# Kernel tuning notes

Measured on AMD Instinct MI355X. Metric: run time of the kernel, lower is better.

The kernel has to match this reference:

```python
import jax, jax.numpy as jnp
import numpy as np

B, T, D, K = 16, 3000, 512, 3
N_TOK = 448          # static max token count (targets are <= 448)
N_MAX = N_TOK + 1    # scatter bins incl. overflow bin, matches torch n_max
LN_EPS = 1e-5


def setup_inputs() -> dict:
    key = jax.random.key(0)
    k0, k1, k2, k3, k4 = jax.random.split(key, 5)
    encoder_1d = jax.random.normal(k0, (B, T, D), jnp.float32)
    # depthwise conv kernel [D, 1, K] (torch Conv1d groups=D, no bias)
    conv_w = jax.random.normal(k1, (D, 1, K), jnp.float32) * (1.0 / np.sqrt(K))
    ln_gamma = jnp.ones((D,), jnp.float32)
    ln_beta = jnp.zeros((D,), jnp.float32)
    proj_w = jax.random.normal(k2, (D,), jnp.float32) * (1.0 / np.sqrt(D))
    alpha_init = min(2048.0 / 3000.0, 0.99)
    proj_b = jnp.float32(np.log(alpha_init / (1.0 - alpha_init)))
    input_lengths = jax.random.randint(k3, (B,), T // 2, T + 1).astype(jnp.int32)
    target_lengths = jax.random.randint(k4, (B,), 300, N_TOK + 1).astype(jnp.int32)
    return {"encoder_1d": encoder_1d, "conv_w": conv_w, "ln_gamma": ln_gamma,
            "ln_beta": ln_beta, "proj_w": proj_w, "proj_b": proj_b,
            "input_lengths": input_lengths, "target_lengths": target_lengths}


def _cif(encoder_1d, conv_w, ln_gamma, ln_beta, proj_w, proj_b,
         input_lengths, target_lengths):
    dt = encoder_1d.dtype
    # ---- weight predictor: depthwise conv + LN + linear + sigmoid ----
    x = jnp.transpose(encoder_1d, (0, 2, 1))                      # [B, D, T]
    x = jax.lax.conv_general_dilated(
        x, conv_w, window_strides=(1,), padding=[(K // 2, K // 2)],
        dimension_numbers=("NCH", "OIH", "NCH"), feature_group_count=D)
    x = jnp.transpose(x, (0, 2, 1))                               # [B, T, D]
    mu = jnp.mean(x, axis=-1, keepdims=True)
    var = jnp.mean(jnp.square(x - mu), axis=-1, keepdims=True)
    x = (x - mu) * jax.lax.rsqrt(var + LN_EPS) * ln_gamma + ln_beta
    alpha = jax.nn.sigmoid(jnp.einsum("btd,d->bt", x, proj_w) + proj_b)  # [B, T]
    # ---- padding mask ----
    valid = jnp.arange(T)[None, :] < input_lengths[:, None]
    alpha = jnp.where(valid, alpha, jnp.zeros((), dt))
    # ---- quantity loss ----
    tgt = target_lengths.astype(dt)
    sum_alpha = jnp.sum(alpha, axis=1)
    qty_loss = jnp.mean(jnp.abs(sum_alpha - tgt))
    # ---- training-mode rescale so cumsum ends exactly at target ----
    alpha_cif = alpha * (tgt / jnp.maximum(sum_alpha, 1e-8))[:, None]
    # ---- CIF integration: cumsum + two scatter-adds ----
    cum = jnp.cumsum(alpha_cif, axis=1)                           # [B, T]
    cum_prev = jnp.pad(cum[:, :-1], ((0, 0), (1, 0)))
    k_lo = jnp.floor(cum_prev).astype(jnp.int32)
    k_hi = jnp.floor(cum).astype(jnp.int32)
    boundary = (k_lo + 1).astype(dt)
    w_lo = jnp.maximum(jnp.minimum(cum, boundary) - cum_prev, 0.0)
    w_hi = jnp.maximum(cum - boundary, 0.0)
    bidx = jnp.arange(B)[:, None]                                 # [B, 1] -> bcast [B, T]
    out = jnp.zeros((B, N_MAX, D), dt)
    out = out.at[bidx, jnp.clip(k_lo, 0, N_MAX - 1)].add(encoder_1d * w_lo[..., None])
    out = out.at[bidx, jnp.clip(k_hi, 0, N_MAX - 1)].add(encoder_1d * w_hi[..., None])
    return out[:, :N_TOK], alpha, qty_loss


def reference(encoder_1d, conv_w, ln_gamma, ln_beta, proj_w, proj_b,
              input_lengths, target_lengths):
    return _cif(encoder_1d, conv_w, ln_gamma, ln_beta, proj_w, proj_b,
                input_lengths, target_lengths)
```

## Files before the change

### kernel.cpp

```cpp
#include <hip/hip_runtime.h>
#include <math.h>

#define B_ 16
#define T_ 3000
#define D_ 512
#define NTOK 448
#define LN_EPS 1e-5f

#define WS_DIFF 16
#define WS_CUM  64
#define WS_AE   (64 + B_ * T_)

struct F8 { float v[8]; };

__device__ inline F8 load8(const float* __restrict__ p) {
    F8 r;
    float4 a = *(const float4*)p;
    float4 b = *(const float4*)(p + 4);
    r.v[0]=a.x; r.v[1]=a.y; r.v[2]=a.z; r.v[3]=a.w;
    r.v[4]=b.x; r.v[5]=b.y; r.v[6]=b.z; r.v[7]=b.w;
    return r;
}

__global__ __launch_bounds__(256) void k_alpha(
    const float* __restrict__ enc, const float* __restrict__ convw,
    const float* __restrict__ gamma, const float* __restrict__ beta,
    const float* __restrict__ projw, const float* __restrict__ projb,
    const int* __restrict__ ilen, float* __restrict__ alpha_out)
{
    const int NB = 188;
    int wave = threadIdx.x >> 6;
    int lane = threadIdx.x & 63;
    int b  = blockIdx.x / NB;
    int tb = blockIdx.x % NB;
    int t0 = tb * 16 + wave * 4;
    int d0 = lane * 8;
    if (t0 >= T_) return;

    int il = ilen[b];
    if (t0 >= il) {
        if (lane == 0) {
#pragma unroll
            for (int q = 0; q < 4; ++q) {
                int t = t0 + q;
                if (t < T_) alpha_out[b * T_ + t] = 0.0f;
            }
        }
        return;
    }

    const float* rowp = enc + ((size_t)b * T_ + t0) * D_ + d0;

    F8 r[6];
#pragma unroll
    for (int i = 0; i < 6; ++i) {
        int t = t0 - 1 + i;
        if (t >= 0 && t < T_) r[i] = load8(rowp + (ptrdiff_t)(i - 1) * D_);
        else { for (int j = 0; j < 8; ++j) r[i].v[j] = 0.f; }
    }

    float w24[24];
    const float4* wp = (const float4*)(convw + (size_t)d0 * 3);
#pragma unroll
    for (int i = 0; i < 6; ++i) {
        float4 q = wp[i];
        w24[4*i+0]=q.x; w24[4*i+1]=q.y; w24[4*i+2]=q.z; w24[4*i+3]=q.w;
    }
    F8 pw = load8(projw + d0);
    F8 gm = load8(gamma + d0);
    F8 bt = load8(beta + d0);
    float pg[8];
    float c0p = 0.f, c1p = 0.f;
#pragma unroll
    for (int j = 0; j < 8; ++j) {
        pg[j] = pw.v[j] * gm.v[j];
        c0p += pw.v[j] * bt.v[j];
        c1p += pg[j];
    }

    float s1[4], s2[4], sp[4];
#pragma unroll
    for (int q = 0; q < 4; ++q) { s1[q]=0.f; s2[q]=0.f; sp[q]=0.f; }

#pragma unroll
    for (int q = 0; q < 4; ++q) {
#pragma unroll
        for (int j = 0; j < 8; ++j) {
            float y = r[q].v[j]*w24[3*j] + r[q+1].v[j]*w24[3*j+1] + r[q+2].v[j]*w24[3*j+2];
            s1[q] += y; s2[q] += y*y; sp[q] += pg[j]*y;
        }
    }
#pragma unroll
    for (int off = 1; off < 64; off <<= 1) {
#pragma unroll
        for (int q = 0; q < 4; ++q) {
            s1[q] += __shfl_xor(s1[q], off);
            s2[q] += __shfl_xor(s2[q], off);
            sp[q] += __shfl_xor(sp[q], off);
        }
        c0p += __shfl_xor(c0p, off);
        c1p += __shfl_xor(c1p, off);
    }
    if (lane == 0) {
        float c0 = c0p + projb[0];
        float c1 = c1p;
#pragma unroll
        for (int q = 0; q < 4; ++q) {
            int t = t0 + q;
            if (t >= T_) break;
            float mu  = s1[q] * (1.0f / D_);
            float var = s2[q] * (1.0f / D_) - mu * mu;
            float rsig = rsqrtf(var + LN_EPS);
            float logit = rsig * (sp[q] - mu * c1) + c0;
            float a = 1.0f / (1.0f + expf(-logit));
            if (t >= il) a = 0.0f;
            alpha_out[b * T_ + t] = a;
        }
    }
}

__global__ __launch_bounds__(512) void k_prep(
    const float* __restrict__ alpha, const int* __restrict__ tlen,
    const int* __restrict__ ilen, float* __restrict__ ws)
{
    __shared__ float sc[T_];
    __shared__ float part[8];
    __shared__ int   sstg[452];

    int b = blockIdx.x;
    int tid = threadIdx.x;
    int wave = tid >> 6;
    int lane = tid & 63;

    float* cumg = ws + WS_CUM + (size_t)b * T_;
    int2*  aeg  = (int2*)(ws + WS_AE) + b * NTOK;

    float run = 0.f;
    for (int base = 0; base < T_; base += 512) {
        int t = base + tid;
        float v = (t < T_) ? alpha[b * T_ + t] : 0.f;
#pragma unroll
        for (int off = 1; off < 64; off <<= 1) {
            float n = __shfl_up(v, off);
            if (lane >= off) v += n;
        }
        if (lane == 63) part[wave] = v;
        __syncthreads();
        float prefix = run;
        for (int w = 0; w < 8; ++w) {
            float pv = part[w];
            if (w < wave) prefix += pv;
            run += pv;
        }
        v += prefix;
        if (t < T_) sc[t] = v;
        __syncthreads();
    }

    float sum = run;
    float tgt = (float)tlen[b];
    float scale = tgt / fmaxf(sum, 1e-8f);
    if (tid == 0) ws[WS_DIFF + b] = fabsf(sum - tgt);

    for (int t = tid; t < T_; t += 512) {
        float cv = sc[t] * scale;
        sc[t] = cv;
        cumg[t] = cv;
    }
    __syncthreads();

    for (int k = tid; k < 450; k += 512) {
        float vk = (float)k;
        int lo = 0, hi = T_;
        while (lo < hi) {
            int mid = (lo + hi) >> 1;
            if (sc[mid] < vk) lo = mid + 1; else hi = mid;
        }
        sstg[k] = lo;
    }
    __syncthreads();

    int il = ilen[b];
    for (int k = tid; k < NTOK; k += 512) {
        int a = sstg[k];
        int e = sstg[k + 1] + 1;
        if (e > il) e = il;
        aeg[k] = make_int2(a, e);
    }
}

__global__ __launch_bounds__(256) void k_gather(
    const float* __restrict__ enc, const float* __restrict__ ws,
    float* __restrict__ out, float* __restrict__ qty)
{
    int bid = blockIdx.x;
    if (bid == B_ * 112) {
        int lane = threadIdx.x;
        if (lane < 64) {
            float v = (lane < B_) ? ws[WS_DIFF + lane] : 0.f;
#pragma unroll
            for (int off = 1; off < 16; off <<= 1) v += __shfl_xor(v, off);
            if (lane == 0) *qty = v * (1.0f / B_);
        }
        return;
    }

    const int NBLK = NTOK / 4;
    int b  = bid / NBLK;
    int kg = bid % NBLK;
    int wave = threadIdx.x >> 6;
    int lane = threadIdx.x & 63;
    int k = kg * 4 + wave;

    const float* cb  = ws + WS_CUM + (size_t)b * T_;
    const int2*  aeg = (const int2*)(ws + WS_AE) + b * NTOK;

    int2 ae = aeg[k];
    int a = ae.x, e = ae.y;

    int d0 = lane * 8;
    const float* encb = enc + (size_t)b * T_ * D_ + d0;

    float4 aa = {0,0,0,0}, ab = {0,0,0,0};
    float fk = (float)k;

    for (int base = a; base < e; base += 63) {
        int n = e - base; if (n > 63) n = 63;
        float cl = 0.0f;
        int t = base - 1 + lane;
        if (lane <= n && t >= 0) cl = cb[t];
        float cn = __shfl_down(cl, 1);
        float fklo = floorf(cl);
        float bnd  = fklo + 1.0f;
        float wlo  = fmaxf(fminf(cn, bnd) - cl, 0.0f);
        float whi  = fmaxf(cn - bnd, 0.0f);
        float wl = (fklo == fk ? wlo : 0.0f) + (floorf(cn) == fk ? whi : 0.0f);
        if (lane >= n) wl = 0.0f;

#pragma unroll 4
        for (int j = 0; j < n; ++j) {
            float w = __shfl(wl, j);
            const float* rp = encb + (size_t)(base + j) * D_;
            float4 ea = *(const float4*)rp;
            float4 eb = *(const float4*)(rp + 4);
            aa.x += ea.x*w; aa.y += ea.y*w; aa.z += ea.z*w; aa.w += ea.w*w;
            ab.x += eb.x*w; ab.y += eb.y*w; ab.z += eb.z*w; ab.w += eb.w*w;
        }
    }

    float* op = out + ((size_t)b * NTOK + k) * D_ + d0;
    *(float4*)op       = aa;
    *(float4*)(op + 4) = ab;
}

extern "C" void kernel_launch(void* const* d_in, const int* in_sizes, int n_in,
                              void* d_out, int out_size, void* d_ws, size_t ws_size,
                              hipStream_t stream) {
    const float* enc   = (const float*)d_in[0];
    const float* convw = (const float*)d_in[1];
    const float* gamma = (const float*)d_in[2];
    const float* beta  = (const float*)d_in[3];
    const float* projw = (const float*)d_in[4];
    const float* projb = (const float*)d_in[5];
    const int*   ilen  = (const int*)d_in[6];
    const int*   tlen  = (const int*)d_in[7];

    float* out_f     = (float*)d_out;
    float* alpha_out = out_f + (size_t)B_ * NTOK * D_;
    float* qty_out   = alpha_out + (size_t)B_ * T_;

    float* ws = (float*)d_ws;

    hipLaunchKernelGGL(k_alpha, dim3(B_ * 188), dim3(256), 0, stream,
                       enc, convw, gamma, beta, projw, projb, ilen, alpha_out);
    hipLaunchKernelGGL(k_prep, dim3(B_), dim3(512), 0, stream,
                       alpha_out, tlen, ilen, ws);
    hipLaunchKernelGGL(k_gather, dim3(B_ * 112 + 1), dim3(256), 0, stream,
                       enc, ws, out_f, qty_out);
}
```

Baseline: 48.07 us.

## Stage conv rows into LDS via async global_load_lds and widen prefix-scan block

```diff
diff --git a/kernel.cpp b/kernel.cpp
--- a/kernel.cpp
+++ b/kernel.cpp
@@ -22,6 +22,12 @@
     return r;
 }
 
+__device__ inline void stage16(const float* src, float* dst) {
+    __builtin_amdgcn_global_load_lds(
+        (const __attribute__((address_space(1))) void*)src,
+        (__attribute__((address_space(3))) void*)dst, 16, 0, 0);
+}
+
 __global__ __launch_bounds__(256) void k_alpha(
     const float* __restrict__ enc, const float* __restrict__ convw,
     const float* __restrict__ gamma, const float* __restrict__ beta,
@@ -29,36 +35,32 @@
     const int* __restrict__ ilen, float* __restrict__ alpha_out)
 {
     const int NB = 188;
-    int wave = threadIdx.x >> 6;
-    int lane = threadIdx.x & 63;
     int b  = blockIdx.x / NB;
     int tb = blockIdx.x % NB;
-    int t0 = tb * 16 + wave * 4;
-    int d0 = lane * 8;
-    if (t0 >= T_) return;
+    int t0 = tb * 16;
+    int tid = threadIdx.x;
+    int wave = tid >> 6;
+    int lane = tid & 63;
 
     int il = ilen[b];
     if (t0 >= il) {
-        if (lane == 0) {
-#pragma unroll
-            for (int q = 0; q < 4; ++q) {
-                int t = t0 + q;
-                if (t < T_) alpha_out[b * T_ + t] = 0.0f;
-            }
-        }
+        int t = t0 + tid;
+        if (tid < 16 && t < T_) alpha_out[b * T_ + t] = 0.0f;
         return;
     }
 
-    const float* rowp = enc + ((size_t)b * T_ + t0) * D_ + d0;
-
-    F8 r[6];
-#pragma unroll
-    for (int i = 0; i < 6; ++i) {
-        int t = t0 - 1 + i;
-        if (t >= 0 && t < T_) r[i] = load8(rowp + (ptrdiff_t)(i - 1) * D_);
-        else { for (int j = 0; j < 8; ++j) r[i].v[j] = 0.f; }
-    }
-
+    __shared__ float lds[18][512];
+
+    const float* encb = enc + (size_t)b * T_ * D_;
+    for (int r = wave; r < 18; r += 4) {
+        int t = t0 - 1 + r;
+        t = t < 0 ? 0 : (t > T_ - 1 ? T_ - 1 : t);
+        const float* src = encb + (size_t)t * D_ + lane * 4;
+        stage16(src,       &lds[r][0]);
+        stage16(src + 256, &lds[r][256]);
+    }
+
+    int d0 = lane * 8;
     float w24[24];
     const float4* wp = (const float4*)(convw + (size_t)d0 * 3);
 #pragma unroll
@@ -78,18 +80,36 @@
         c1p += pg[j];
     }
 
+    __syncthreads();
+
+    int w4 = wave * 4;
+    float4 ra0 = *(const float4*)&lds[w4][d0];
+    float4 ra1 = *(const float4*)&lds[w4][d0 + 4];
+    float4 rb0 = *(const float4*)&lds[w4 + 1][d0];
+    float4 rb1 = *(const float4*)&lds[w4 + 1][d0 + 4];
+
     float s1[4], s2[4], sp[4];
 #pragma unroll
     for (int q = 0; q < 4; ++q) { s1[q]=0.f; s2[q]=0.f; sp[q]=0.f; }
 
 #pragma unroll
     for (int q = 0; q < 4; ++q) {
+        float4 rc0 = *(const float4*)&lds[w4 + q + 2][d0];
+        float4 rc1 = *(const float4*)&lds[w4 + q + 2][d0 + 4];
+        int t = t0 + w4 + q;
+        float m0 = (t == 0)      ? 0.f : 1.f;
+        float m2 = (t >= T_ - 1) ? 0.f : 1.f;
+        float xm[8] = {ra0.x,ra0.y,ra0.z,ra0.w, ra1.x,ra1.y,ra1.z,ra1.w};
+        float xc[8] = {rb0.x,rb0.y,rb0.z,rb0.w, rb1.x,rb1.y,rb1.z,rb1.w};
+        float xp[8] = {rc0.x,rc0.y,rc0.z,rc0.w, rc1.x,rc1.y,rc1.z,rc1.w};
 #pragma unroll
         for (int j = 0; j < 8; ++j) {
-            float y = r[q].v[j]*w24[3*j] + r[q+1].v[j]*w24[3*j+1] + r[q+2].v[j]*w24[3*j+2];
+            float y = (xm[j]*m0)*w24[3*j] + xc[j]*w24[3*j+1] + (xp[j]*m2)*w24[3*j+2];
             s1[q] += y; s2[q] += y*y; sp[q] += pg[j]*y;
         }
-    }
+        ra0 = rb0; ra1 = rb1; rb0 = rc0; rb1 = rc1;
+    }
+
 #pragma unroll
     for (int off = 1; off < 64; off <<= 1) {
 #pragma unroll
@@ -106,7 +126,7 @@
         float c1 = c1p;
 #pragma unroll
         for (int q = 0; q < 4; ++q) {
-            int t = t0 + q;
+            int t = t0 + w4 + q;
             if (t >= T_) break;
             float mu  = s1[q] * (1.0f / D_);
             float var = s2[q] * (1.0f / D_) - mu * mu;
@@ -119,12 +139,12 @@
     }
 }
 
-__global__ __launch_bounds__(512) void k_prep(
+__global__ __launch_bounds__(1024) void k_prep(
     const float* __restrict__ alpha, const int* __restrict__ tlen,
     const int* __restrict__ ilen, float* __restrict__ ws)
 {
     __shared__ float sc[T_];
-    __shared__ float part[8];
+    __shared__ float part[16];
     __shared__ int   sstg[452];
 
     int b = blockIdx.x;
@@ -136,7 +156,7 @@
     int2*  aeg  = (int2*)(ws + WS_AE) + b * NTOK;
 
     float run = 0.f;
-    for (int base = 0; base < T_; base += 512) {
+    for (int base = 0; base < T_; base += 1024) {
         int t = base + tid;
         float v = (t < T_) ? alpha[b * T_ + t] : 0.f;
 #pragma unroll
@@ -147,7 +167,7 @@
         if (lane == 63) part[wave] = v;
         __syncthreads();
         float prefix = run;
-        for (int w = 0; w < 8; ++w) {
+        for (int w = 0; w < 16; ++w) {
             float pv = part[w];
             if (w < wave) prefix += pv;
             run += pv;
@@ -162,30 +182,30 @@
     float scale = tgt / fmaxf(sum, 1e-8f);
     if (tid == 0) ws[WS_DIFF + b] = fabsf(sum - tgt);
 
-    for (int t = tid; t < T_; t += 512) {
+    for (int t = tid; t < T_; t += 1024) {
         float cv = sc[t] * scale;
         sc[t] = cv;
         cumg[t] = cv;
     }
     __syncthreads();
 
-    for (int k = tid; k < 450; k += 512) {
-        float vk = (float)k;
+    if (tid < 450) {
+        float vk = (float)tid;
         int lo = 0, hi = T_;
         while (lo < hi) {
             int mid = (lo + hi) >> 1;
             if (sc[mid] < vk) lo = mid + 1; else hi = mid;
         }
-        sstg[k] = lo;
+        sstg[tid] = lo;
     }
     __syncthreads();
 
     int il = ilen[b];
-    for (int k = tid; k < NTOK; k += 512) {
-        int a = sstg[k];
-        int e = sstg[k + 1] + 1;
+    if (tid < NTOK) {
+        int a = sstg[tid];
+        int e = sstg[tid + 1] + 1;
         if (e > il) e = il;
-        aeg[k] = make_int2(a, e);
+        aeg[tid] = make_int2(a, e);
     }
 }
 
@@ -273,7 +293,7 @@
 
     hipLaunchKernelGGL(k_alpha, dim3(B_ * 188), dim3(256), 0, stream,
                        enc, convw, gamma, beta, projw, projb, ilen, alpha_out);
-    hipLaunchKernelGGL(k_prep, dim3(B_), dim3(512), 0, stream,
+    hipLaunchKernelGGL(k_prep, dim3(B_), dim3(1024), 0, stream,
                        alpha_out, tlen, ilen, ws);
     hipLaunchKernelGGL(k_gather, dim3(B_ * 112 + 1), dim3(256), 0, stream,
                        enc, ws, out_f, qty_out);
```

Measured after the change: 47.20 us. Within noise of the previous version (-1.8%).
